# Performance work log

Measured on AMD Instinct MI355X. Metric: run time of the kernel, lower is better.

The kernel has to match this reference:

```python
import jax, jax.numpy as jnp
import numpy as np

EPS = 1e-5  # torch nn.LayerNorm default

def setup_inputs() -> dict:
    key = jax.random.key(0)
    k1, k2 = jax.random.split(key)
    x = jax.random.normal(k1, (8388608, 4), dtype=jnp.float32)
    W = jax.random.normal(k2, (4, 3), dtype=jnp.float32)
    gamma = jnp.ones((4,), dtype=jnp.float32)
    beta = jnp.zeros((4,), dtype=jnp.float32)
    return {"x": x, "W": W, "gamma": gamma, "beta": beta}

def reference(x, W, gamma, beta):
    # LayerNorm over last dim (size 4)
    mu = jnp.mean(x, axis=-1, keepdims=True)
    var = jnp.mean(jnp.square(x - mu), axis=-1, keepdims=True)
    h = (x - mu) * jax.lax.rsqrt(var + EPS) * gamma + beta
    # small linear (4 -> 3) then softmax over last dim
    logits = h @ W  # [N, 3]
    return jax.nn.softmax(logits, axis=-1)
```

## Files before the change

kernel.cpp:

```cpp
#include <hip/hip_runtime.h>

#define LN_EPS 1e-5f

typedef float v4f __attribute__((ext_vector_type(4)));

constexpr int BLOCK = 256;
constexpr int RPT   = 4;
constexpr int RPB   = BLOCK * RPT;

__global__ __launch_bounds__(BLOCK) void ln_linear_softmax_kernel(
    const v4f*   __restrict__ x,
    const float* __restrict__ W,
    const float* __restrict__ gamma,
    const float* __restrict__ beta,
    v4f*         __restrict__ out4,
    int n)
{
    __shared__ float lds[RPB * 3];

    const int  tid  = threadIdx.x;
    const long base = (long)blockIdx.x * RPB;

    const v4f g = *(const v4f*)gamma;
    const v4f b = *(const v4f*)beta;
    const v4f* W4 = (const v4f*)W;
    const v4f w0 = W4[0];
    const v4f w1 = W4[1];
    const v4f w2 = W4[2];

    v4f v[RPT];

    if (base + RPB <= (long)n) {
        #pragma unroll
        for (int k = 0; k < RPT; ++k)
            v[k] = __builtin_nontemporal_load(&x[base + tid + k * BLOCK]);

        #pragma unroll
        for (int k = 0; k < RPT; ++k) {
            const int rl = tid + k * BLOCK;
            v4f q = v[k];

            float mu = (q.x + q.y + q.z + q.w) * 0.25f;
            float dx = q.x - mu, dy = q.y - mu, dz = q.z - mu, dw = q.w - mu;
            float var = (dx*dx + dy*dy + dz*dz + dw*dw) * 0.25f;
            float rs  = rsqrtf(var + LN_EPS);

            float h0 = dx * rs * g.x + b.x;
            float h1 = dy * rs * g.y + b.y;
            float h2 = dz * rs * g.z + b.z;
            float h3 = dw * rs * g.w + b.w;

            float l0 = h0*w0.x + h1*w0.w + h2*w1.z + h3*w2.y;
            float l1 = h0*w0.y + h1*w1.x + h2*w1.w + h3*w2.z;
            float l2 = h0*w0.z + h1*w1.y + h2*w2.x + h3*w2.w;

            float m   = fmaxf(l0, fmaxf(l1, l2));
            float e0  = __expf(l0 - m);
            float e1  = __expf(l1 - m);
            float e2  = __expf(l2 - m);
            float inv = 1.0f / (e0 + e1 + e2);

            lds[rl*3 + 0] = e0 * inv;
            lds[rl*3 + 1] = e1 * inv;
            lds[rl*3 + 2] = e2 * inv;
        }
    } else {
        #pragma unroll
        for (int k = 0; k < RPT; ++k) {
            const int  rl  = tid + k * BLOCK;
            const long row = base + rl;
            if (row < n) {
                v4f q = __builtin_nontemporal_load(&x[row]);

                float mu = (q.x + q.y + q.z + q.w) * 0.25f;
                float dx = q.x - mu, dy = q.y - mu, dz = q.z - mu, dw = q.w - mu;
                float var = (dx*dx + dy*dy + dz*dz + dw*dw) * 0.25f;
                float rs  = rsqrtf(var + LN_EPS);

                float h0 = dx * rs * g.x + b.x;
                float h1 = dy * rs * g.y + b.y;
                float h2 = dz * rs * g.z + b.z;
                float h3 = dw * rs * g.w + b.w;

                float l0 = h0*w0.x + h1*w0.w + h2*w1.z + h3*w2.y;
                float l1 = h0*w0.y + h1*w1.x + h2*w1.w + h3*w2.z;
                float l2 = h0*w0.z + h1*w1.y + h2*w2.x + h3*w2.w;

                float m   = fmaxf(l0, fmaxf(l1, l2));
                float e0  = __expf(l0 - m);
                float e1  = __expf(l1 - m);
                float e2  = __expf(l2 - m);
                float inv = 1.0f / (e0 + e1 + e2);

                lds[rl*3 + 0] = e0 * inv;
                lds[rl*3 + 1] = e1 * inv;
                lds[rl*3 + 2] = e2 * inv;
            }
        }
    }

    __syncthreads();

    const v4f* lds4  = (const v4f*)lds;
    const long obase = (long)blockIdx.x * (RPB * 3 / 4);
    const long on4   = ((long)n * 3) / 4;
    #pragma unroll
    for (int k = 0; k < 3; ++k) {
        const long oi = obase + tid + k * BLOCK;
        if (oi < on4) {
            __builtin_nontemporal_store(lds4[tid + k * BLOCK], &out4[oi]);
        }
    }
}

extern "C" void kernel_launch(void* const* d_in, const int* in_sizes, int n_in,
                              void* d_out, int out_size, void* d_ws, size_t ws_size,
                              hipStream_t stream) {
    const float* x     = (const float*)d_in[0];
    const float* W     = (const float*)d_in[1];
    const float* gamma = (const float*)d_in[2];
    const float* beta  = (const float*)d_in[3];
    v4f* out4 = (v4f*)d_out;

    int n = in_sizes[0] / 4;
    int grid = (n + RPB - 1) / RPB;
    ln_linear_softmax_kernel<<<grid, BLOCK, 0, stream>>>(
        (const v4f*)x, W, gamma, beta, out4, n);
}
```

Before: 213.4 us.

## Make LDS output staging per-wavefront and drop block-wide barrier

Each 64-lane wavefront now owns a contiguous chunk of 256 rows and its own LDS region, so the output transpose through LDS only needs an s_waitcnt instead of a __syncthreads. The block size is doubled to 512. The tail path writes scalar outputs directly to global memory and skips LDS entirely. Wavefronts can then drain their stores independently rather than waiting on the whole block. The cost is a little more LDS per block and reliance on wavefront-synchronous LDS visibility.

```diff
diff --git a/kernel.cpp b/kernel.cpp
--- a/kernel.cpp
+++ b/kernel.cpp
@@ -4,8 +4,9 @@
 
 typedef float v4f __attribute__((ext_vector_type(4)));
 
-constexpr int BLOCK = 256;
+constexpr int BLOCK = 512;
 constexpr int RPT   = 4;
+constexpr int WROWS = 64 * RPT;
 constexpr int RPB   = BLOCK * RPT;
 
 __global__ __launch_bounds__(BLOCK) void ln_linear_softmax_kernel(
@@ -18,8 +19,11 @@
 {
     __shared__ float lds[RPB * 3];
 
-    const int  tid  = threadIdx.x;
-    const long base = (long)blockIdx.x * RPB;
+    const int  tid   = threadIdx.x;
+    const int  wid   = tid >> 6;
+    const int  lane  = tid & 63;
+    const long base  = (long)blockIdx.x * RPB;
+    const long wbase = base + (long)wid * WROWS;
 
     const v4f g = *(const v4f*)gamma;
     const v4f b = *(const v4f*)beta;
@@ -28,16 +32,17 @@
     const v4f w1 = W4[1];
     const v4f w2 = W4[2];
 
-    v4f v[RPT];
+    float* wlds = &lds[wid * (WROWS * 3)];
 
     if (base + RPB <= (long)n) {
+        v4f v[RPT];
         #pragma unroll
         for (int k = 0; k < RPT; ++k)
-            v[k] = __builtin_nontemporal_load(&x[base + tid + k * BLOCK]);
+            v[k] = __builtin_nontemporal_load(&x[wbase + lane + 64 * k]);
 
         #pragma unroll
         for (int k = 0; k < RPT; ++k) {
-            const int rl = tid + k * BLOCK;
+            const int rl = lane + 64 * k;
             v4f q = v[k];
 
             float mu = (q.x + q.y + q.z + q.w) * 0.25f;
@@ -60,15 +65,24 @@
             float e2  = __expf(l2 - m);
             float inv = 1.0f / (e0 + e1 + e2);
 
-            lds[rl*3 + 0] = e0 * inv;
-            lds[rl*3 + 1] = e1 * inv;
-            lds[rl*3 + 2] = e2 * inv;
+            wlds[rl*3 + 0] = e0 * inv;
+            wlds[rl*3 + 1] = e1 * inv;
+            wlds[rl*3 + 2] = e2 * inv;
+        }
+
+        asm volatile("s_waitcnt lgkmcnt(0)" ::: "memory");
+
+        const v4f* wlds4 = (const v4f*)wlds;
+        const long ow4   = (wbase * 3) >> 2;
+        #pragma unroll
+        for (int k = 0; k < 3; ++k) {
+            __builtin_nontemporal_store(wlds4[lane + 64 * k],
+                                        &out4[ow4 + lane + 64 * k]);
         }
     } else {
-        #pragma unroll
+        float* out = (float*)out4;
         for (int k = 0; k < RPT; ++k) {
-            const int  rl  = tid + k * BLOCK;
-            const long row = base + rl;
+            const long row = wbase + lane + 64 * k;
             if (row < n) {
                 v4f q = __builtin_nontemporal_load(&x[row]);
 
@@ -92,23 +106,10 @@
                 float e2  = __expf(l2 - m);
                 float inv = 1.0f / (e0 + e1 + e2);
 
-                lds[rl*3 + 0] = e0 * inv;
-                lds[rl*3 + 1] = e1 * inv;
-                lds[rl*3 + 2] = e2 * inv;
+                out[row*3 + 0] = e0 * inv;
+                out[row*3 + 1] = e1 * inv;
+                out[row*3 + 2] = e2 * inv;
             }
-        }
-    }
-
-    __syncthreads();
-
-    const v4f* lds4  = (const v4f*)lds;
-    const long obase = (long)blockIdx.x * (RPB * 3 / 4);
-    const long on4   = ((long)n * 3) / 4;
-    #pragma unroll
-    for (int k = 0; k < 3; ++k) {
-        const long oi = obase + tid + k * BLOCK;
-        if (oi < on4) {
-            __builtin_nontemporal_store(lds4[tid + k * BLOCK], &out4[oi]);
         }
     }
 }
```

Result: no change. 213.7 us (+0.1%).
